# Kernel tuning notes

Hardware: AMD Instinct MI355X
Metric: run time of the kernel (lower is better)

## Reference

```python
import jax, jax.numpy as jnp
import numpy as np

NV, NE, H, P = 50000, 10000, 256, 400000

def setup_inputs() -> dict:
    key = jax.random.key(0)
    ks = jax.random.split(key, 16)
    s = 1.0 / np.sqrt(H)
    return {
        "v": jax.random.normal(ks[0], (NV, H), jnp.float32),
        "e": jax.random.normal(ks[1], (NE, H), jnp.float32),
        "W_v2e_w": jax.random.normal(ks[2], (H, H), jnp.float32) * s,
        "W_v2e_b": jnp.zeros((H,), jnp.float32),
        "W_e2v_w": jax.random.normal(ks[3], (H, H), jnp.float32) * s,
        "W_e2v_b": jnp.zeros((H,), jnp.float32),
        "n_weight": jax.random.uniform(ks[4], (NV, 1), jnp.float32),
        "e_weight": jax.random.uniform(ks[5], (NE, 1), jnp.float32),
        "n_reg_weight": jax.random.uniform(ks[6], (P, 1), jnp.float32),
        "e_reg_weight": jax.random.uniform(ks[7], (P, 1), jnp.float32),
        "e_reg_sum": jax.random.uniform(ks[8], (NE, 1), jnp.float32) + 1.0,  # positive normalizer
        "n_reg_sum": jax.random.uniform(ks[9], (NV, 1), jnp.float32) + 1.0,
        "pairs_v": jax.random.randint(ks[10], (P,), 0, NV, jnp.int32),  # ve_lists[:,0]
        "eidx": jax.random.randint(ks[11], (P,), 0, NE, jnp.int32),
        "pairs_e": jax.random.randint(ks[12], (P,), 0, NE, jnp.int32),  # ve_lists[:,1]
        "vidx": jax.random.randint(ks[13], (P,), 0, NV, jnp.int32),
    }

def reference(v, e, W_v2e_w, W_v2e_b, W_e2v_w, W_e2v_b, n_weight, e_weight,
              n_reg_weight, e_reg_weight, e_reg_sum, n_reg_sum,
              pairs_v, eidx, pairs_e, vidx):
    # v2e: dense transform on vertices, gather per incidence, scatter-add into edges
    ve = jax.nn.relu(v @ W_v2e_w.T + W_v2e_b)            # [NV,H]
    v_acc = v * n_weight                                 # v *= n_weight * v_fac(=1)
    msg_ve = (ve * n_weight)[pairs_v] * n_reg_weight     # [P,H]
    e_out = e.at[eidx].add(msg_ve) / e_reg_sum           # [NE,H]
    # e2v: dense transform on edges, gather per incidence, scatter-add into vertices
    ev = jax.nn.relu(e_out @ W_e2v_w.T + W_e2v_b)        # [NE,H]
    msg_ev = (ev * e_weight)[pairs_e] * e_reg_weight     # [P,H]
    v_out = v_acc.at[vidx].add(msg_ev) / n_reg_sum       # [NV,H]
    return v_out, e_out
```

## Files before the change

### kernel.cpp

```cpp
#include <hip/hip_runtime.h>
#include <stdint.h>

#define NV 50000
#define NE 10000
#define HD 256
#define NP 400000

#define SE 128
#define SV 48

#define PREP_FBLK ((NP + 255) / 256)
#define PREP_WBLK 64
#define PREP_VBLK 6250

typedef short short8 __attribute__((ext_vector_type(8)));
typedef short short4v __attribute__((ext_vector_type(4)));
typedef float f32x4 __attribute__((ext_vector_type(4)));

__device__ __forceinline__ short f2bf(float f) {
    unsigned int u = __builtin_bit_cast(unsigned int, f);
    u += 0x7FFFu + ((u >> 16) & 1u);
    return (short)(u >> 16);
}
__device__ __forceinline__ float bf2f(short s) {
    unsigned int u = ((unsigned int)(unsigned short)s) << 16;
    return __builtin_bit_cast(float, u);
}

__global__ __launch_bounds__(256) void prep_kernel(
    const float* __restrict__ v, const float* __restrict__ W1, const float* __restrict__ W2,
    const int* __restrict__ eidx, const int* __restrict__ vidx,
    short* __restrict__ v_bf, short* __restrict__ W_bf,
    int* __restrict__ cnt_e, int* __restrict__ cnt_v,
    int* __restrict__ bkt_e, int* __restrict__ bkt_v, int conv_v)
{
    int b = blockIdx.x;
    int tid = threadIdx.x;
    if (b < PREP_FBLK) {
        int p = b * 256 + tid;
        if (p < NP) {
            int er = eidx[p];
            int vr = vidx[p];
            int se = atomicAdd(&cnt_e[er], 1);
            if (se < SE) bkt_e[er * SE + se] = p;
            int sv = atomicAdd(&cnt_v[vr], 1);
            if (sv < SV) bkt_v[vr * SV + sv] = p;
        }
    } else if (b < PREP_FBLK + PREP_WBLK) {
        size_t i = (size_t)(b - PREP_FBLK) * 2048 + (size_t)tid * 8;
        const float* src = (i < 65536) ? (W1 + i) : (W2 + (i - 65536));
        float4 a0 = *(const float4*)src;
        float4 a1 = *(const float4*)(src + 4);
        short8 s;
        s[0] = f2bf(a0.x); s[1] = f2bf(a0.y); s[2] = f2bf(a0.z); s[3] = f2bf(a0.w);
        s[4] = f2bf(a1.x); s[5] = f2bf(a1.y); s[6] = f2bf(a1.z); s[7] = f2bf(a1.w);
        *(short8*)(W_bf + i) = s;
    } else {
        if (!conv_v) return;
        size_t i = (size_t)(b - PREP_FBLK - PREP_WBLK) * 2048 + (size_t)tid * 8;
        float4 a0 = *(const float4*)(v + i);
        float4 a1 = *(const float4*)(v + i + 4);
        short8 s;
        s[0] = f2bf(a0.x); s[1] = f2bf(a0.y); s[2] = f2bf(a0.z); s[3] = f2bf(a0.w);
        s[4] = f2bf(a1.x); s[5] = f2bf(a1.y); s[6] = f2bf(a1.z); s[7] = f2bf(a1.w);
        *(short8*)(v_bf + i) = s;
    }
}

__global__ __launch_bounds__(256) void gemm_rs(
    const void* __restrict__ Av, int a_bf,
    const short* __restrict__ Wb,
    const float* __restrict__ bias,
    const float* __restrict__ rowscale,
    short* __restrict__ out,
    int M)
{
    __shared__ short As[64 * 256];
    __shared__ short Ws[64 * 256];
    const int tid  = threadIdx.x;
    const int row0 = blockIdx.x * 64;

#pragma unroll
    for (int it = 0; it < 8; ++it) {
        int cl = it * 256 + tid;
        int r  = cl >> 5;
        int c  = cl & 31;
        int gr = row0 + r; gr = gr < M ? gr : M - 1;
        short8 ap;
        if (a_bf) {
            ap = *(const short8*)((const short*)Av + (size_t)gr * HD + (c << 3));
        } else {
            const float* asrc = (const float*)Av + (size_t)gr * HD + (c << 3);
            float4 a0 = *(const float4*)asrc;
            float4 a1 = *(const float4*)(asrc + 4);
            ap[0] = f2bf(a0.x); ap[1] = f2bf(a0.y); ap[2] = f2bf(a0.z); ap[3] = f2bf(a0.w);
            ap[4] = f2bf(a1.x); ap[5] = f2bf(a1.y); ap[6] = f2bf(a1.z); ap[7] = f2bf(a1.w);
        }
        *(short8*)&As[(r << 8) + ((c ^ (r & 7)) << 3)] = ap;
    }

    const int lane = tid & 63;
    const int wv   = tid >> 6;
    const int m16  = lane & 15;
    const int quad = lane >> 4;
    const int arow = (wv << 4) + m16;

    for (int ct = 0; ct < 4; ++ct) {
        __syncthreads();
#pragma unroll
        for (int it = 0; it < 8; ++it) {
            int cl = it * 256 + tid;
            int r  = cl >> 5;
            int c  = cl & 31;
            short8 wp = *(const short8*)(Wb + (size_t)((ct << 6) + r) * HD + (c << 3));
            *(short8*)&Ws[(r << 8) + ((c ^ (r & 7)) << 3)] = wp;
        }
        __syncthreads();

        f32x4 acc[4];
#pragma unroll
        for (int nt = 0; nt < 4; ++nt) acc[nt] = (f32x4){0.f, 0.f, 0.f, 0.f};

#pragma unroll
        for (int ks = 0; ks < 8; ++ks) {
            int c = (ks << 2) + quad;
            short8 afr = *(const short8*)&As[(arow << 8) + ((c ^ (arow & 7)) << 3)];
#pragma unroll
            for (int nt = 0; nt < 4; ++nt) {
                int brow = (nt << 4) + m16;
                short8 bfr = *(const short8*)&Ws[(brow << 8) + ((c ^ (m16 & 7)) << 3)];
                acc[nt] = __builtin_amdgcn_mfma_f32_16x16x32_bf16(afr, bfr, acc[nt], 0, 0, 0);
            }
        }

#pragma unroll
        for (int r = 0; r < 4; ++r) {
            int row = row0 + (wv << 4) + (quad << 2) + r;
            if (row < M) {
                float rs = rowscale[row];
#pragma unroll
                for (int nt = 0; nt < 4; ++nt) {
                    int col = (ct << 6) + (nt << 4) + m16;
                    float val = acc[nt][r] + bias[col];
                    val = fmaxf(val, 0.0f) * rs;
                    out[(size_t)row * HD + col] = f2bf(val);
                }
            }
        }
    }
}

__device__ __forceinline__ void gather_core(
    const short* __restrict__ msg, const int* __restrict__ perm,
    const int* __restrict__ pairs, const float* __restrict__ regw,
    int i, int end, int lane, float4& acc)
{
    while (i < end) {
        int n = end - i; n = n < 64 ? n : 64;
        int src = 0; float w = 0.f;
        if (lane < n) {
            int p = perm[i + lane];
            src = pairs[p];
            w = regw[p];
        }
        int j = 0;
        for (; j + 4 <= n; j += 4) {
            int   s0 = __shfl(src, j),     s1 = __shfl(src, j + 1);
            int   s2 = __shfl(src, j + 2), s3 = __shfl(src, j + 3);
            float w0 = __shfl(w, j),       w1 = __shfl(w, j + 1);
            float w2 = __shfl(w, j + 2),   w3 = __shfl(w, j + 3);
            short4v m0 = *(const short4v*)(msg + ((size_t)s0 << 8) + (lane << 2));
            short4v m1 = *(const short4v*)(msg + ((size_t)s1 << 8) + (lane << 2));
            short4v m2 = *(const short4v*)(msg + ((size_t)s2 << 8) + (lane << 2));
            short4v m3 = *(const short4v*)(msg + ((size_t)s3 << 8) + (lane << 2));
            acc.x += bf2f(m0[0]) * w0; acc.y += bf2f(m0[1]) * w0;
            acc.z += bf2f(m0[2]) * w0; acc.w += bf2f(m0[3]) * w0;
            acc.x += bf2f(m1[0]) * w1; acc.y += bf2f(m1[1]) * w1;
            acc.z += bf2f(m1[2]) * w1; acc.w += bf2f(m1[3]) * w1;
            acc.x += bf2f(m2[0]) * w2; acc.y += bf2f(m2[1]) * w2;
            acc.z += bf2f(m2[2]) * w2; acc.w += bf2f(m2[3]) * w2;
            acc.x += bf2f(m3[0]) * w3; acc.y += bf2f(m3[1]) * w3;
            acc.z += bf2f(m3[2]) * w3; acc.w += bf2f(m3[3]) * w3;
        }
        for (; j < n; ++j) {
            int s0 = __shfl(src, j); float w0 = __shfl(w, j);
            short4v m0 = *(const short4v*)(msg + ((size_t)s0 << 8) + (lane << 2));
            acc.x += bf2f(m0[0]) * w0; acc.y += bf2f(m0[1]) * w0;
            acc.z += bf2f(m0[2]) * w0; acc.w += bf2f(m0[3]) * w0;
        }
        i += n;
    }
}

__global__ __launch_bounds__(256) void gather_e(
    const short* __restrict__ msg,
    const int* __restrict__ bkt,
    const int* __restrict__ cnt,
    const int* __restrict__ pairs, const float* __restrict__ regw,
    const float* __restrict__ e_in, const float* __restrict__ reg_sum,
    float* __restrict__ out, short* __restrict__ out_bf)
{
    int r    = (blockIdx.x << 2) + (threadIdx.x >> 6);
    int lane = threadIdx.x & 63;
    float4 acc = ((const float4*)(e_in + (size_t)r * HD))[lane];
    int n = cnt[r]; n = n < SE ? n : SE;
    int i0 = r * SE;
    gather_core(msg, bkt, pairs, regw, i0, i0 + n, lane, acc);
    float inv = 1.0f / reg_sum[r];
    acc.x *= inv; acc.y *= inv; acc.z *= inv; acc.w *= inv;
    ((float4*)(out + (size_t)r * HD))[lane] = acc;
    if (out_bf) {
        short4v s;
        s[0] = f2bf(acc.x); s[1] = f2bf(acc.y); s[2] = f2bf(acc.z); s[3] = f2bf(acc.w);
        *(short4v*)(out_bf + (size_t)r * HD + (lane << 2)) = s;
    }
}

__global__ __launch_bounds__(256) void gather_v(
    const short* __restrict__ msg,
    const int* __restrict__ bkt,
    const int* __restrict__ cnt,
    const int* __restrict__ pairs, const float* __restrict__ regw,
    const float* __restrict__ v_f32, const short* __restrict__ v_bf,
    const float* __restrict__ n_w,
    const float* __restrict__ reg_sum, float* __restrict__ out)
{
    int r    = (blockIdx.x << 2) + (threadIdx.x >> 6);
    int lane = threadIdx.x & 63;
    float nw = n_w[r];
    float4 a;
    if (v_bf) {
        short4v b = *(const short4v*)(v_bf + (size_t)r * HD + (lane << 2));
        a.x = bf2f(b[0]); a.y = bf2f(b[1]); a.z = bf2f(b[2]); a.w = bf2f(b[3]);
    } else {
        a = ((const float4*)(v_f32 + (size_t)r * HD))[lane];
    }
    float4 acc; acc.x = a.x * nw; acc.y = a.y * nw; acc.z = a.z * nw; acc.w = a.w * nw;
    int n = cnt[r]; n = n < SV ? n : SV;
    int i0 = r * SV;
    gather_core(msg, bkt, pairs, regw, i0, i0 + n, lane, acc);
    float inv = 1.0f / reg_sum[r];
    acc.x *= inv; acc.y *= inv; acc.z *= inv; acc.w *= inv;
    ((float4*)(out + (size_t)r * HD))[lane] = acc;
}

extern "C" void kernel_launch(void* const* d_in, const int* in_sizes, int n_in,
                              void* d_out, int out_size, void* d_ws, size_t ws_size,
                              hipStream_t stream) {
    const float* v   = (const float*)d_in[0];
    const float* e   = (const float*)d_in[1];
    const float* W1  = (const float*)d_in[2];
    const float* b1  = (const float*)d_in[3];
    const float* W2  = (const float*)d_in[4];
    const float* b2  = (const float*)d_in[5];
    const float* n_weight     = (const float*)d_in[6];
    const float* e_weight     = (const float*)d_in[7];
    const float* n_reg_weight = (const float*)d_in[8];
    const float* e_reg_weight = (const float*)d_in[9];
    const float* e_reg_sum    = (const float*)d_in[10];
    const float* n_reg_sum    = (const float*)d_in[11];
    const int* pairs_v = (const int*)d_in[12];
    const int* eidx    = (const int*)d_in[13];
    const int* pairs_e = (const int*)d_in[14];
    const int* vidx    = (const int*)d_in[15];

    float* out      = (float*)d_out;
    float* v_region = out;
    float* e_region = out + (size_t)NV * HD;

    char* ws = (char*)d_ws;
    size_t o = 0;
    short* msg     = (short*)(ws + o); o += (size_t)NV * HD * 2;
    int*   bkt_e   = (int*)(ws + o);   o += (size_t)NE * SE * 4;
    int*   bkt_v   = (int*)(ws + o);   o += (size_t)NV * SV * 4;
    short* W_bf    = (short*)(ws + o); o += (size_t)2 * 65536 * 2;
    int*   cnt_e   = (int*)(ws + o);   o += (size_t)NE * 4;
    int*   cnt_v   = (int*)(ws + o);   o += (size_t)NV * 4;
    size_t o_opt = o;
    short* e_bf    = (short*)(ws + o_opt);
    short* v_bf    = (short*)(ws + o_opt + (size_t)NE * HD * 2);
    size_t need_ebf  = o_opt + (size_t)NE * HD * 2;
    size_t need_full = need_ebf + (size_t)NV * HD * 2;
    const int has_ebf = (ws_size >= need_ebf);
    const int full    = (ws_size >= need_full);

    hipMemsetAsync(cnt_e, 0, (size_t)(NE + NV) * 4, stream);
    prep_kernel<<<PREP_FBLK + PREP_WBLK + PREP_VBLK, 256, 0, stream>>>(
        v, W1, W2, eidx, vidx, full ? v_bf : (short*)msg , W_bf,
        cnt_e, cnt_v, bkt_e, bkt_v, full);

    gemm_rs<<<(NV + 63) / 64, 256, 0, stream>>>(
        full ? (const void*)v_bf : (const void*)v, full, W_bf, b1, n_weight, msg, NV);
    gather_e<<<NE / 4, 256, 0, stream>>>(msg, bkt_e, cnt_e,
        pairs_v, n_reg_weight, e, e_reg_sum, e_region, has_ebf ? e_bf : (short*)0);
    gemm_rs<<<(NE + 63) / 64, 256, 0, stream>>>(
        has_ebf ? (const void*)e_bf : (const void*)e_region, has_ebf, W_bf + 65536, b2, e_weight, msg, NE);
    gather_v<<<NV / 4, 256, 0, stream>>>(msg, bkt_v, cnt_v,
        pairs_e, e_reg_weight, v, full ? v_bf : (short*)0, n_weight, n_reg_sum, v_region);
}
```

Before: 305.1 us.

## Build incidence buckets with chunked LDS byte-packed histograms instead of global atomics

Replaces the per-incidence global atomic bucketing with a few large blocks that each take a chunk of the pair list and count into shared-memory histograms packed four 8-bit counters per word. Edge buckets are split into per-chunk sub-buckets with per-chunk counts. Vertex buckets reserve their global offsets with one atomic per nonzero counter and then fill slots through LDS atomics. The goal is to cut global atomic contention. In exchange the bucketing runs on only 8 blocks, which limits parallelism, and 8-bit counters plus 40-slot sub-buckets could overflow for high-degree rows. The conversion blocks are also resized to 1024 threads.

Result: slower. 413.4 us (+35.5%).

```diff
diff --git a/kernel.cpp b/kernel.cpp
--- a/kernel.cpp
+++ b/kernel.cpp
@@ -6,12 +6,16 @@
 #define HD 256
 #define NP 400000
 
-#define SE 128
-#define SV 48
-
-#define PREP_FBLK ((NP + 255) / 256)
-#define PREP_WBLK 64
-#define PREP_VBLK 6250
+#define SVB 48
+#define SEB 160
+#define SUB_E 40
+#define NCH 4
+#define CHUNK (NP / NCH)
+
+#define FB_E NCH
+#define FB_V NCH
+#define PREP_WBLK 16
+#define PREP_VBLK 1563
 
 typedef short short8 __attribute__((ext_vector_type(8)));
 typedef short short4v __attribute__((ext_vector_type(4)));
@@ -27,27 +31,65 @@
     return __builtin_bit_cast(float, u);
 }
 
-__global__ __launch_bounds__(256) void prep_kernel(
+__global__ __launch_bounds__(1024) void prep_kernel(
     const float* __restrict__ v, const float* __restrict__ W1, const float* __restrict__ W2,
     const int* __restrict__ eidx, const int* __restrict__ vidx,
     short* __restrict__ v_bf, short* __restrict__ W_bf,
-    int* __restrict__ cnt_e, int* __restrict__ cnt_v,
+    int* __restrict__ cnt_v,
+    int* __restrict__ cnt_e2,
     int* __restrict__ bkt_e, int* __restrict__ bkt_v, int conv_v)
 {
+    __shared__ int h[12500];
     int b = blockIdx.x;
     int tid = threadIdx.x;
-    if (b < PREP_FBLK) {
-        int p = b * 256 + tid;
-        if (p < NP) {
+    if (b < FB_E) {
+        for (int w = tid; w < 2500; w += 1024) h[w] = 0;
+        __syncthreads();
+        int base = b * CHUNK;
+        for (int p = base + tid; p < base + CHUNK; p += 1024) {
             int er = eidx[p];
+            int sh = (er & 3) * 8;
+            unsigned old = atomicAdd((unsigned*)&h[er >> 2], 1u << sh);
+            int slot = (old >> sh) & 0xFF;
+            if (slot < SUB_E) bkt_e[er * SEB + b * SUB_E + slot] = p;
+        }
+        __syncthreads();
+        for (int r = tid; r < NE; r += 1024)
+            cnt_e2[b * NE + r] = (h[r >> 2] >> ((r & 3) * 8)) & 0xFF;
+    } else if (b < FB_E + FB_V) {
+        int c = b - FB_E;
+        for (int w = tid; w < 12500; w += 1024) h[w] = 0;
+        __syncthreads();
+        int base = c * CHUNK;
+        for (int p = base + tid; p < base + CHUNK; p += 1024) {
             int vr = vidx[p];
-            int se = atomicAdd(&cnt_e[er], 1);
-            if (se < SE) bkt_e[er * SE + se] = p;
-            int sv = atomicAdd(&cnt_v[vr], 1);
-            if (sv < SV) bkt_v[vr * SV + sv] = p;
-        }
-    } else if (b < PREP_FBLK + PREP_WBLK) {
-        size_t i = (size_t)(b - PREP_FBLK) * 2048 + (size_t)tid * 8;
+            atomicAdd((unsigned*)&h[vr >> 2], 1u << ((vr & 3) * 8));
+        }
+        __syncthreads();
+        for (int w = tid; w < 12500; w += 1024) {
+            unsigned x = (unsigned)h[w];
+            if (x) {
+                unsigned y = 0;
+#pragma unroll
+                for (int k = 0; k < 4; ++k) {
+                    unsigned c8 = (x >> (k * 8)) & 0xFFu;
+                    unsigned s = 0;
+                    if (c8) s = (unsigned)atomicAdd(&cnt_v[w * 4 + k], (int)c8);
+                    y |= (s & 0xFFu) << (k * 8);
+                }
+                h[w] = (int)y;
+            }
+        }
+        __syncthreads();
+        for (int p = base + tid; p < base + CHUNK; p += 1024) {
+            int vr = vidx[p];
+            int sh = (vr & 3) * 8;
+            unsigned old = atomicAdd((unsigned*)&h[vr >> 2], 1u << sh);
+            int slot = (old >> sh) & 0xFF;
+            if (slot < SVB) bkt_v[vr * SVB + slot] = p;
+        }
+    } else if (b < FB_E + FB_V + PREP_WBLK) {
+        size_t i = (size_t)(b - FB_E - FB_V) * 8192 + (size_t)tid * 8;
         const float* src = (i < 65536) ? (W1 + i) : (W2 + (i - 65536));
         float4 a0 = *(const float4*)src;
         float4 a1 = *(const float4*)(src + 4);
@@ -57,7 +99,8 @@
         *(short8*)(W_bf + i) = s;
     } else {
         if (!conv_v) return;
-        size_t i = (size_t)(b - PREP_FBLK - PREP_WBLK) * 2048 + (size_t)tid * 8;
+        size_t i = (size_t)(b - FB_E - FB_V - PREP_WBLK) * 8192 + (size_t)tid * 8;
+        if (i >= (size_t)NV * HD) return;
         float4 a0 = *(const float4*)(v + i);
         float4 a1 = *(const float4*)(v + i + 4);
         short8 s;
@@ -203,9 +246,12 @@
     int r    = (blockIdx.x << 2) + (threadIdx.x >> 6);
     int lane = threadIdx.x & 63;
     float4 acc = ((const float4*)(e_in + (size_t)r * HD))[lane];
-    int n = cnt[r]; n = n < SE ? n : SE;
-    int i0 = r * SE;
-    gather_core(msg, bkt, pairs, regw, i0, i0 + n, lane, acc);
+#pragma unroll
+    for (int c = 0; c < NCH; ++c) {
+        int n = cnt[c * NE + r]; n = n < SUB_E ? n : SUB_E;
+        int i0 = r * SEB + c * SUB_E;
+        gather_core(msg, bkt, pairs, regw, i0, i0 + n, lane, acc);
+    }
     float inv = 1.0f / reg_sum[r];
     acc.x *= inv; acc.y *= inv; acc.z *= inv; acc.w *= inv;
     ((float4*)(out + (size_t)r * HD))[lane] = acc;
@@ -236,8 +282,8 @@
         a = ((const float4*)(v_f32 + (size_t)r * HD))[lane];
     }
     float4 acc; acc.x = a.x * nw; acc.y = a.y * nw; acc.z = a.z * nw; acc.w = a.w * nw;
-    int n = cnt[r]; n = n < SV ? n : SV;
-    int i0 = r * SV;
+    int n = cnt[r]; n = n < SVB ? n : SVB;
+    int i0 = r * SVB;
     gather_core(msg, bkt, pairs, regw, i0, i0 + n, lane, acc);
     float inv = 1.0f / reg_sum[r];
     acc.x *= inv; acc.y *= inv; acc.z *= inv; acc.w *= inv;
@@ -271,10 +317,10 @@
     char* ws = (char*)d_ws;
     size_t o = 0;
     short* msg     = (short*)(ws + o); o += (size_t)NV * HD * 2;
-    int*   bkt_e   = (int*)(ws + o);   o += (size_t)NE * SE * 4;
-    int*   bkt_v   = (int*)(ws + o);   o += (size_t)NV * SV * 4;
+    int*   bkt_e   = (int*)(ws + o);   o += (size_t)NE * SEB * 4;
+    int*   bkt_v   = (int*)(ws + o);   o += (size_t)NV * SVB * 4;
     short* W_bf    = (short*)(ws + o); o += (size_t)2 * 65536 * 2;
-    int*   cnt_e   = (int*)(ws + o);   o += (size_t)NE * 4;
+    int*   cnt_e2  = (int*)(ws + o);   o += (size_t)NCH * NE * 4;
     int*   cnt_v   = (int*)(ws + o);   o += (size_t)NV * 4;
     size_t o_opt = o;
     short* e_bf    = (short*)(ws + o_opt);
@@ -284,14 +330,14 @@
     const int has_ebf = (ws_size >= need_ebf);
     const int full    = (ws_size >= need_full);
 
-    hipMemsetAsync(cnt_e, 0, (size_t)(NE + NV) * 4, stream);
-    prep_kernel<<<PREP_FBLK + PREP_WBLK + PREP_VBLK, 256, 0, stream>>>(
+    hipMemsetAsync(cnt_v, 0, (size_t)NV * 4, stream);
+    prep_kernel<<<FB_E + FB_V + PREP_WBLK + PREP_VBLK, 1024, 0, stream>>>(
         v, W1, W2, eidx, vidx, full ? v_bf : (short*)msg , W_bf,
-        cnt_e, cnt_v, bkt_e, bkt_v, full);
+        cnt_v, cnt_e2, bkt_e, bkt_v, full);
 
     gemm_rs<<<(NV + 63) / 64, 256, 0, stream>>>(
         full ? (const void*)v_bf : (const void*)v, full, W_bf, b1, n_weight, msg, NV);
-    gather_e<<<NE / 4, 256, 0, stream>>>(msg, bkt_e, cnt_e,
+    gather_e<<<NE / 4, 256, 0, stream>>>(msg, bkt_e, cnt_e2,
         pairs_v, n_reg_weight, e, e_reg_sum, e_region, has_ebf ? e_bf : (short*)0);
     gemm_rs<<<(NE + 63) / 64, 256, 0, stream>>>(
         has_ebf ? (const void*)e_bf : (const void*)e_region, has_ebf, W_bf + 65536, b2, e_weight, msg, NE);
```

## Replace global-atomic bucketing with chunked LDS histograms, scan, and placement

Applied to the files above, without the earlier changes.

Builds the incidence buckets in three steps instead of one. First, 64 chunks each count edge and vertex row occurrences into shared-memory histograms, packing four 8-bit counters per int. A per-row scan over chunks then produces the offsets, and a placement kernel replays each chunk with LDS atomics to write bucket slots. This removes 800k contended global atomics and the memset, and the bucket order becomes deterministic. The costs are two extra launches, a 60KB LDS footprint that also applies to the bf16 conversion blocks in the prep kernel, and 8-bit counters that would overflow if any row's total count exceeded 255. The histogram scratch reuses the e_bf buffer, and e_bf is now always used.

New measurement: 291.6 us. 4.4% less time.

```diff
diff --git a/kernel.cpp b/kernel.cpp
--- a/kernel.cpp
+++ b/kernel.cpp
@@ -9,9 +9,14 @@
 #define SE 128
 #define SV 48
 
-#define PREP_FBLK ((NP + 255) / 256)
-#define PREP_WBLK 64
-#define PREP_VBLK 6250
+#define NCH 64
+#define CHP (NP / NCH)
+#define NR  60000
+#define NW  15000
+
+#define PREP_HBLK NCH
+#define PREP_WBLK 16
+#define PREP_VBLK 1563
 
 typedef short short8 __attribute__((ext_vector_type(8)));
 typedef short short4v __attribute__((ext_vector_type(4)));
@@ -27,27 +32,31 @@
     return __builtin_bit_cast(float, u);
 }
 
-__global__ __launch_bounds__(256) void prep_kernel(
+__global__ __launch_bounds__(1024) void prep_kernel(
     const float* __restrict__ v, const float* __restrict__ W1, const float* __restrict__ W2,
     const int* __restrict__ eidx, const int* __restrict__ vidx,
     short* __restrict__ v_bf, short* __restrict__ W_bf,
-    int* __restrict__ cnt_e, int* __restrict__ cnt_v,
-    int* __restrict__ bkt_e, int* __restrict__ bkt_v, int conv_v)
-{
+    int* __restrict__ cnt8,
+    int conv_v)
+{
+    __shared__ int h[NW];
     int b = blockIdx.x;
     int tid = threadIdx.x;
-    if (b < PREP_FBLK) {
-        int p = b * 256 + tid;
-        if (p < NP) {
+    if (b < PREP_HBLK) {
+        for (int w = tid; w < NW; w += 1024) h[w] = 0;
+        __syncthreads();
+        int base = b * CHP;
+        for (int k = tid; k < CHP; k += 1024) {
+            int p = base + k;
             int er = eidx[p];
-            int vr = vidx[p];
-            int se = atomicAdd(&cnt_e[er], 1);
-            if (se < SE) bkt_e[er * SE + se] = p;
-            int sv = atomicAdd(&cnt_v[vr], 1);
-            if (sv < SV) bkt_v[vr * SV + sv] = p;
-        }
-    } else if (b < PREP_FBLK + PREP_WBLK) {
-        size_t i = (size_t)(b - PREP_FBLK) * 2048 + (size_t)tid * 8;
+            atomicAdd((unsigned*)&h[er >> 2], 1u << ((er & 3) * 8));
+            int rv = 10000 + vidx[p];
+            atomicAdd((unsigned*)&h[rv >> 2], 1u << ((rv & 3) * 8));
+        }
+        __syncthreads();
+        for (int w = tid; w < NW; w += 1024) cnt8[b * NW + w] = h[w];
+    } else if (b < PREP_HBLK + PREP_WBLK) {
+        size_t i = (size_t)(b - PREP_HBLK) * 8192 + (size_t)tid * 8;
         const float* src = (i < 65536) ? (W1 + i) : (W2 + (i - 65536));
         float4 a0 = *(const float4*)src;
         float4 a1 = *(const float4*)(src + 4);
@@ -57,13 +66,57 @@
         *(short8*)(W_bf + i) = s;
     } else {
         if (!conv_v) return;
-        size_t i = (size_t)(b - PREP_FBLK - PREP_WBLK) * 2048 + (size_t)tid * 8;
+        size_t i = (size_t)(b - PREP_HBLK - PREP_WBLK) * 8192 + (size_t)tid * 8;
+        if (i >= (size_t)NV * HD) return;
         float4 a0 = *(const float4*)(v + i);
         float4 a1 = *(const float4*)(v + i + 4);
         short8 s;
         s[0] = f2bf(a0.x); s[1] = f2bf(a0.y); s[2] = f2bf(a0.z); s[3] = f2bf(a0.w);
         s[4] = f2bf(a1.x); s[5] = f2bf(a1.y); s[6] = f2bf(a1.z); s[7] = f2bf(a1.w);
         *(short8*)(v_bf + i) = s;
+    }
+}
+
+__global__ __launch_bounds__(256) void scan_kernel(
+    int* __restrict__ cnt8, int* __restrict__ cnt_e, int* __restrict__ cnt_v)
+{
+    int w = blockIdx.x * 256 + threadIdx.x;
+    if (w >= NW) return;
+    unsigned acc = 0;
+#pragma unroll 4
+    for (int c = 0; c < NCH; ++c) {
+        unsigned x = (unsigned)cnt8[c * NW + w];
+        cnt8[c * NW + w] = (int)acc;
+        acc += x;
+    }
+    int r0 = w * 4;
+    int4 t;
+    t.x = acc & 0xFF; t.y = (acc >> 8) & 0xFF; t.z = (acc >> 16) & 0xFF; t.w = acc >> 24;
+    if (r0 < 10000) *(int4*)&cnt_e[r0] = t;
+    else            *(int4*)&cnt_v[r0 - 10000] = t;
+}
+
+__global__ __launch_bounds__(1024) void place_kernel(
+    const int* __restrict__ eidx, const int* __restrict__ vidx,
+    const int* __restrict__ cnt8,
+    int* __restrict__ bkt_e, int* __restrict__ bkt_v)
+{
+    __shared__ int h[NW];
+    int c = blockIdx.x;
+    int tid = threadIdx.x;
+    for (int w = tid; w < NW; w += 1024) h[w] = cnt8[c * NW + w];
+    __syncthreads();
+    int base = c * CHP;
+    for (int k = tid; k < CHP; k += 1024) {
+        int p = base + k;
+        int er = eidx[p];
+        unsigned old = atomicAdd((unsigned*)&h[er >> 2], 1u << ((er & 3) * 8));
+        int s = (old >> ((er & 3) * 8)) & 0xFF;
+        if (s < SE) bkt_e[er * SE + s] = p;
+        int rv = 10000 + vidx[p];
+        old = atomicAdd((unsigned*)&h[rv >> 2], 1u << ((rv & 3) * 8));
+        s = (old >> ((rv & 3) * 8)) & 0xFF;
+        if (s < SV) bkt_v[(rv - 10000) * SV + s] = p;
     }
 }
 
@@ -274,27 +327,27 @@
     int*   bkt_e   = (int*)(ws + o);   o += (size_t)NE * SE * 4;
     int*   bkt_v   = (int*)(ws + o);   o += (size_t)NV * SV * 4;
     short* W_bf    = (short*)(ws + o); o += (size_t)2 * 65536 * 2;
+    int*   cnt8    = (int*)(ws + o);
+    short* e_bf    = (short*)(ws + o); o += (size_t)NE * HD * 2;
     int*   cnt_e   = (int*)(ws + o);   o += (size_t)NE * 4;
     int*   cnt_v   = (int*)(ws + o);   o += (size_t)NV * 4;
     size_t o_opt = o;
-    short* e_bf    = (short*)(ws + o_opt);
-    short* v_bf    = (short*)(ws + o_opt + (size_t)NE * HD * 2);
-    size_t need_ebf  = o_opt + (size_t)NE * HD * 2;
-    size_t need_full = need_ebf + (size_t)NV * HD * 2;
-    const int has_ebf = (ws_size >= need_ebf);
-    const int full    = (ws_size >= need_full);
-
-    hipMemsetAsync(cnt_e, 0, (size_t)(NE + NV) * 4, stream);
-    prep_kernel<<<PREP_FBLK + PREP_WBLK + PREP_VBLK, 256, 0, stream>>>(
+    short* v_bf    = (short*)(ws + o_opt);
+    size_t need_full = o_opt + (size_t)NV * HD * 2;
+    const int full = (ws_size >= need_full);
+
+    prep_kernel<<<PREP_HBLK + PREP_WBLK + PREP_VBLK, 1024, 0, stream>>>(
         v, W1, W2, eidx, vidx, full ? v_bf : (short*)msg , W_bf,
-        cnt_e, cnt_v, bkt_e, bkt_v, full);
+        cnt8, full);
+    scan_kernel<<<(NW + 255) / 256, 256, 0, stream>>>(cnt8, cnt_e, cnt_v);
+    place_kernel<<<NCH, 1024, 0, stream>>>(eidx, vidx, cnt8, bkt_e, bkt_v);
 
     gemm_rs<<<(NV + 63) / 64, 256, 0, stream>>>(
         full ? (const void*)v_bf : (const void*)v, full, W_bf, b1, n_weight, msg, NV);
     gather_e<<<NE / 4, 256, 0, stream>>>(msg, bkt_e, cnt_e,
-        pairs_v, n_reg_weight, e, e_reg_sum, e_region, has_ebf ? e_bf : (short*)0);
+        pairs_v, n_reg_weight, e, e_reg_sum, e_region, e_bf);
     gemm_rs<<<(NE + 63) / 64, 256, 0, stream>>>(
-        has_ebf ? (const void*)e_bf : (const void*)e_region, has_ebf, W_bf + 65536, b2, e_weight, msg, NE);
+        (const void*)e_bf, 1, W_bf + 65536, b2, e_weight, msg, NE);
     gather_v<<<NV / 4, 256, 0, stream>>>(msg, bkt_v, cnt_v,
         pairs_e, e_reg_weight, v, full ? v_bf : (short*)0, n_weight, n_reg_sum, v_region);
 }
```
